# Performance work log

Measured on AMD Instinct MI355X. Metric: run time of the kernel, lower is better.

Reference implementation:

```python
import jax, jax.numpy as jnp
import numpy as np

B, L, E, H = 4, 2048, 512, 8


def setup_inputs() -> dict:
    key = jax.random.key(0)
    ks = jax.random.split(key, 12)
    s = 0.02
    inp = {
        "values": jax.random.normal(ks[0], (B, L, E), jnp.float32),
        "keys": jax.random.normal(ks[1], (B, L, E), jnp.float32),
        "queries": jax.random.normal(ks[2], (B, L, E), jnp.float32),
    }
    mask = jax.random.randint(ks[3], (B, L, H, H), 0, 2, jnp.int32)
    # guarantee at least one unmasked entry per softmax row to avoid NaN rows
    mask = mask.at[..., 0].set(1)
    inp["mask"] = mask
    # Linear(E, E*H) weights stored as (in, out); torch uses y = x @ W.T + b
    inp["Wv"] = jax.random.normal(ks[4], (E, E * H), jnp.float32) * s
    inp["bv"] = jnp.zeros((E * H,), jnp.float32)
    inp["Wk"] = jax.random.normal(ks[5], (E, E * H), jnp.float32) * s
    inp["bk"] = jnp.zeros((E * H,), jnp.float32)
    inp["Wq"] = jax.random.normal(ks[6], (E, E * H), jnp.float32) * s
    inp["bq"] = jnp.zeros((E * H,), jnp.float32)
    inp["Wo"] = jax.random.normal(ks[7], (E * H, E), jnp.float32) * s
    inp["bo"] = jnp.zeros((E,), jnp.float32)
    return inp


def reference(values, keys, queries, mask, Wv, bv, Wk, bk, Wq, bq, Wo, bo):
    b, l, e = queries.shape
    h = Wq.shape[1] // e

    def proj(x, W, bias):
        # (B,L,E) -> (B,L,H,E) -> transpose(1,2) -> (B,H,L,E)
        return (x @ W + bias).reshape(b, -1, h, e).transpose(0, 2, 1, 3)

    v = proj(values, Wv, bv)
    k = proj(keys, Wk, bk)
    q = proj(queries, Wq, bq)
    # Faithful to source: einsum labels applied to the TRANSPOSED (B,H,L,E)
    # tensors, so 'q'/'k' bind to the heads axis and 'h' binds to seq axis.
    # energy: (B, L, H, H) -- head-vs-head scores at each position.
    energy = jnp.einsum('nqhd,nkhd->nhqk', q, k)
    energy = jnp.where(mask == 0, -jnp.inf, energy)
    attn = jax.nn.softmax(energy / jnp.sqrt(jnp.float32(e)), axis=3)
    # out of einsum: (B, H, L, E); raw row-major reshape to (B, L, H*E)
    out = jnp.einsum('nhql,nlhd->nqhd', attn, v).reshape(b, -1, h * e)
    return out @ Wo + bo
```

## Files before the change

### kernel.cpp

```cpp
#include <hip/hip_runtime.h>
#include <stdint.h>

typedef __attribute__((ext_vector_type(4))) float f32x4;
typedef __attribute__((ext_vector_type(8))) __bf16 bf16x8;

__device__ __forceinline__ unsigned short f2bf(float f) {
  union { float f; uint32_t u; } v; v.f = f;
  uint32_t u = v.u;
  return (unsigned short)((u + 0x7FFFu + ((u >> 16) & 1u)) >> 16);
}
__device__ __forceinline__ float bflo(uint32_t u) {
  union { uint32_t u; float f; } v; v.u = u << 16; return v.f;
}
__device__ __forceinline__ float bfhi(uint32_t u) {
  union { uint32_t u; float f; } v; v.u = u & 0xffff0000u; return v.f;
}

__device__ __forceinline__ void async_copy16(void* lds, const void* g) {
  __builtin_amdgcn_global_load_lds(
      (const __attribute__((address_space(1))) void*)g,
      (__attribute__((address_space(3))) void*)lds,
      16, 0, 0);
}

__global__ void cvt3_f32_bf16(const float* __restrict__ in0,
                              const float* __restrict__ in1,
                              const float* __restrict__ in2,
                              uint32_t* __restrict__ out, int n) {
  const float* in = (blockIdx.y == 0) ? in0 : (blockIdx.y == 1) ? in1 : in2;
  uint32_t* o = out + (size_t)blockIdx.y * (n / 2);
  int i = blockIdx.x * blockDim.x + threadIdx.x;
  int idx = i * 8;
  if (idx >= n) return;
  float4 a = *(const float4*)(in + idx);
  float4 b = *(const float4*)(in + idx + 4);
  uint4 ov;
  ov.x = f2bf(a.x) | ((uint32_t)f2bf(a.y) << 16);
  ov.y = f2bf(a.z) | ((uint32_t)f2bf(a.w) << 16);
  ov.z = f2bf(b.x) | ((uint32_t)f2bf(b.y) << 16);
  ov.w = f2bf(b.z) | ((uint32_t)f2bf(b.w) << 16);
  *(uint4*)(o + i * 4) = ov;
}

__global__ void transpose3_to_bf16(const float* __restrict__ in0,
                                   const float* __restrict__ in1,
                                   const float* __restrict__ in2,
                                   unsigned short* __restrict__ out,
                                   int R, int C) {
  const float* in = (blockIdx.z == 0) ? in0 : (blockIdx.z == 1) ? in1 : in2;
  unsigned short* o = out + (size_t)blockIdx.z * ((size_t)R * C);
  __shared__ float tile[32][33];
  int c0 = blockIdx.x * 32, r0 = blockIdx.y * 32;
  int tx = threadIdx.x, ty = threadIdx.y;
  #pragma unroll
  for (int rr = 0; rr < 32; rr += 8)
    tile[ty + rr][tx] = in[(size_t)(r0 + ty + rr) * C + c0 + tx];
  __syncthreads();
  #pragma unroll
  for (int rr = 0; rr < 32; rr += 8)
    o[(size_t)(c0 + ty + rr) * R + r0 + tx] = f2bf(tile[tx][ty + rr]);
}

__global__ void transpose_to_bf16(const float* __restrict__ in,
                                  unsigned short* __restrict__ out,
                                  int R, int C) {
  __shared__ float tile[32][33];
  int c0 = blockIdx.x * 32, r0 = blockIdx.y * 32;
  int tx = threadIdx.x, ty = threadIdx.y;
  #pragma unroll
  for (int rr = 0; rr < 32; rr += 8)
    tile[ty + rr][tx] = in[(size_t)(r0 + ty + rr) * C + c0 + tx];
  __syncthreads();
  #pragma unroll
  for (int rr = 0; rr < 32; rr += 8)
    out[(size_t)(c0 + ty + rr) * R + r0 + tx] = f2bf(tile[tx][ty + rr]);
}

template <int NK, int NN, bool PARTIAL, bool DUAL>
__global__ __launch_bounds__(512, 2) void gemm256(
    const unsigned short* __restrict__ A,
    const unsigned short* __restrict__ Bt,
    const float* __restrict__ bias,
    void* __restrict__ Cout,
    const unsigned short* __restrict__ A2,
    const unsigned short* __restrict__ Bt2,
    const float* __restrict__ bias2,
    void* __restrict__ Cout2,
    int Mt, int NtG, int KC, int Kfull) {
  constexpr int TT = NK * NN;
  static_assert(TT >= 4 && (TT % 2) == 0, "need even TT >= 4");
  __shared__ unsigned short lds[2 * 2 * 256 * 64];

  const int nwg = Mt * NtG * KC;
  const int cpx = nwg >> 3;
  const int bid = blockIdx.x;
  const int nb = (bid & 7) * cpx + (bid >> 3);
  const int kc = nb / (Mt * NtG);
  const int r2 = nb % (Mt * NtG);
  const int bm = r2 / NtG;
  const int ng = r2 % NtG;
  const int mat = DUAL ? (ng >> 3) : 0;
  const int ngm = DUAL ? (ng & 7) : ng;
  const int N = (DUAL ? (NtG >> 1) : NtG) * NN * 256;
  const size_t koff = (size_t)kc * (NK * 64);

  const unsigned short* Asrc = (DUAL && mat) ? A2 : A;
  const unsigned short* Bsrc = (DUAL && mat) ? Bt2 : Bt;
  const float* biasd = (DUAL && mat) ? bias2 : bias;
  void* Cd = (DUAL && mat) ? Cout2 : Cout;

  const int tid = threadIdx.x;
  const int wv = tid >> 6, ln = tid & 63;
  const int wm = wv >> 2, wn = wv & 3;

  f32x4 acc[8][4] = {};
  bf16x8 af[4][2];
  bf16x8 bfb[2][2];

  char* const lds0 = (char*)lds;
  char* const lds1 = (char*)lds + 65536;

  auto stage_tile = [&](int tt, char* dst) {
    const int kt = tt % NK;
    const int bnn = ngm * NN + tt / NK;
    #pragma unroll
    for (int i = 0; i < 4; ++i) {
      const int rb = i * 64 + wv * 8;
      const int row = rb + (ln >> 3);
      const int kcs = (ln & 7) ^ (row & 7);
      async_copy16(dst + rb * 128,
                   Asrc + (size_t)(bm * 256 + row) * Kfull + koff + kt * 64 + kcs * 8);
      async_copy16(dst + 32768 + rb * 128,
                   Bsrc + (size_t)(bnn * 256 + row) * Kfull + koff + kt * 64 + kcs * 8);
    }
  };
  auto load_af = [&](int mh, const char* buf) {
    #pragma unroll
    for (int f = 0; f < 4; ++f) {
      const int lr = wm * 128 + (mh * 4 + f) * 16 + (ln & 15);
      #pragma unroll
      for (int s = 0; s < 2; ++s) {
        const int kq = s * 4 + (ln >> 4);
        af[f][s] = *(const bf16x8*)(buf + lr * 128 + ((kq ^ (lr & 7)) * 16));
      }
    }
  };
  auto load_bf = [&](int nh, const char* buf) {
    #pragma unroll
    for (int gq = 0; gq < 2; ++gq) {
      const int lr = wn * 64 + (nh * 2 + gq) * 16 + (ln & 15);
      #pragma unroll
      for (int s = 0; s < 2; ++s) {
        const int kq = s * 4 + (ln >> 4);
        bfb[gq][s] =
            *(const bf16x8*)(buf + 32768 + lr * 128 + ((kq ^ (lr & 7)) * 16));
      }
    }
  };
  auto mfma_quad = [&](int mh, int nh) {
    #pragma unroll
    for (int s = 0; s < 2; ++s)
      #pragma unroll
      for (int f = 0; f < 4; ++f)
        #pragma unroll
        for (int gq = 0; gq < 2; ++gq)
          acc[mh * 4 + f][nh * 2 + gq] = __builtin_amdgcn_mfma_f32_16x16x32_bf16(
              bfb[gq][s], af[f][s], acc[mh * 4 + f][nh * 2 + gq], 0, 0, 0);
  };
  auto epilogue = [&](int nt) {
    const int m0 = bm * 256 + wm * 128 + (ln & 15);
    const int n0 = (ngm * NN + nt) * 256 + wn * 64 + ((ln >> 4) << 2);
    if (PARTIAL) {
      float* Cp = (float*)Cd + (size_t)kc * ((size_t)Mt * 256) * N;
      #pragma unroll
      for (int f = 0; f < 8; ++f) {
        const int row = m0 + f * 16;
        #pragma unroll
        for (int g = 0; g < 4; ++g)
          *(f32x4*)(Cp + (size_t)row * N + n0 + g * 16) = acc[f][g];
      }
    } else {
      unsigned short* C = (unsigned short*)Cd;
      #pragma unroll
      for (int f = 0; f < 8; ++f) {
        const int row = m0 + f * 16;
        #pragma unroll
        for (int g = 0; g < 4; ++g) {
          const int col = n0 + g * 16;
          float4 bv = *(const float4*)(biasd + col);
          uint2 o;
          o.x = f2bf(acc[f][g][0] + bv.x) | ((uint32_t)f2bf(acc[f][g][1] + bv.y) << 16);
          o.y = f2bf(acc[f][g][2] + bv.z) | ((uint32_t)f2bf(acc[f][g][3] + bv.w) << 16);
          *(uint2*)(C + (size_t)row * N + col) = o;
        }
      }
    }
    #pragma unroll
    for (int f = 0; f < 8; ++f)
      #pragma unroll
      for (int g = 0; g < 4; ++g)
        acc[f][g] = (f32x4){0.f, 0.f, 0.f, 0.f};
  };

  auto tile_body = [&](int tau, const char* buf, char* obuf) {
    if (tau + 1 < TT) stage_tile(tau + 1, obuf);
    load_af(0, buf); load_bf(0, buf);
    mfma_quad(0, 0);
    load_bf(1, buf);
    mfma_quad(0, 1);
    load_af(1, buf);
    mfma_quad(1, 1);
    load_bf(0, buf);
    mfma_quad(1, 0);
    __builtin_amdgcn_sched_barrier(0);
    if (tau + 1 < TT)
      asm volatile("s_waitcnt vmcnt(0)" ::: "memory");
    __builtin_amdgcn_s_barrier();
    if ((tau + 1) % NK == 0) epilogue(tau / NK);
  };

  stage_tile(0, lds0);
  asm volatile("s_waitcnt vmcnt(0)" ::: "memory");
  __builtin_amdgcn_sched_barrier(0);
  __builtin_amdgcn_s_barrier();

  for (int it = 0; it < TT / 2; ++it) {
    tile_body(2 * it,     lds0, lds1);
    tile_body(2 * it + 1, lds1, lds0);
  }
}

__global__ void reduce4_bias(const float* __restrict__ p,
                             const float* __restrict__ bo,
                             float* __restrict__ out) {
  const size_t S = (size_t)8192 * 512;
  size_t i = ((size_t)blockIdx.x * 256 + threadIdx.x) * 4;
  float4 a = *(const float4*)(p + i);
  float4 b = *(const float4*)(p + S + i);
  float4 c = *(const float4*)(p + 2 * S + i);
  float4 d = *(const float4*)(p + 3 * S + i);
  float4 bb = *(const float4*)(bo + (int)(i & 511));
  float4 o;
  o.x = a.x + b.x + c.x + d.x + bb.x;
  o.y = a.y + b.y + c.y + d.y + bb.y;
  o.z = a.z + b.z + c.z + d.z + bb.z;
  o.w = a.w + b.w + c.w + d.w + bb.w;
  *(float4*)(out + i) = o;
}

__global__ __launch_bounds__(256) void energy_mfma(
    const unsigned short* __restrict__ Q,
    const unsigned short* __restrict__ Kb,
    const int* __restrict__ mask,
    float* __restrict__ P) {
  const int wave = threadIdx.x >> 6, ln = threadIdx.x & 63;
  const int t2 = (blockIdx.x * 4 + wave) * 2;
  const int r16 = ln & 15;
  const int g = ln >> 4;
  const size_t rowoff = (size_t)(t2 + (r16 >> 3)) * 4096 + (r16 & 7) * 512 + g * 8;
  const unsigned short* qb = Q + rowoff;
  const unsigned short* kb = Kb + rowoff;

  f32x4 acc = {};
  #pragma unroll
  for (int s = 0; s < 16; ++s) {
    bf16x8 qf = *(const bf16x8*)(qb + s * 32);
    bf16x8 kf = *(const bf16x8*)(kb + s * 32);
    acc = __builtin_amdgcn_mfma_f32_16x16x32_bf16(qf, kf, acc, 0, 0, 0);
  }

  const int ct = r16 >> 3, j = r16 & 7;
  const bool valid = ((g >> 1) == ct);
  const int tok = t2 + ct;
  float pv[4];
  #pragma unroll
  for (int r = 0; r < 4; ++r) {
    const int i = (g & 1) * 4 + r;
    float e = acc[r] * 0.044194173824159216f;
    int mk = 1;
    if (valid) mk = mask[(size_t)tok * 64 + i * 8 + j];
    if (mk == 0) e = -1e30f;
    float m = e;
    m = fmaxf(m, __shfl_xor(m, 1, 64));
    m = fmaxf(m, __shfl_xor(m, 2, 64));
    m = fmaxf(m, __shfl_xor(m, 4, 64));
    float p = __expf(e - m);
    float sum = p;
    sum += __shfl_xor(sum, 1, 64);
    sum += __shfl_xor(sum, 2, 64);
    sum += __shfl_xor(sum, 4, 64);
    pv[r] = p / sum;
  }
  if (valid) {
    #pragma unroll
    for (int r = 0; r < 4; ++r) {
      const int i = (g & 1) * 4 + r;
      P[(size_t)tok * 64 + i * 8 + j] = pv[r];
    }
  }
}

__global__ __launch_bounds__(256) void pv_kernel(
    const float* __restrict__ P,
    const unsigned short* __restrict__ Vb,
    unsigned short* __restrict__ out2) {
  const int wave = threadIdx.x >> 6, lane = threadIdx.x & 63;
  const int t = blockIdx.x * 4 + wave;
  const unsigned short* Vr = Vb + (size_t)t * 4096;
  float att = P[(size_t)t * 64 + lane];

  uint4 v4[8];
  #pragma unroll
  for (int jj = 0; jj < 8; ++jj)
    v4[jj] = *(const uint4*)(Vr + jj * 512 + lane * 8);

  const int nb = t >> 11, l = t & 2047;
  const size_t tok_base = (size_t)nb * 8388608 + (size_t)(l >> 3) * 4096 +
                          (size_t)(l & 7) * 512 + lane * 8;
  #pragma unroll
  for (int hh = 0; hh < 8; ++hh) {
    float accv[8] = {0.f, 0.f, 0.f, 0.f, 0.f, 0.f, 0.f, 0.f};
    #pragma unroll
    for (int jj = 0; jj < 8; ++jj) {
      float a = __shfl(att, hh * 8 + jj, 64);
      accv[0] += a * bflo(v4[jj].x); accv[1] += a * bfhi(v4[jj].x);
      accv[2] += a * bflo(v4[jj].y); accv[3] += a * bfhi(v4[jj].y);
      accv[4] += a * bflo(v4[jj].z); accv[5] += a * bfhi(v4[jj].z);
      accv[6] += a * bflo(v4[jj].w); accv[7] += a * bfhi(v4[jj].w);
    }
    uint4 o;
    o.x = f2bf(accv[0]) | ((uint32_t)f2bf(accv[1]) << 16);
    o.y = f2bf(accv[2]) | ((uint32_t)f2bf(accv[3]) << 16);
    o.z = f2bf(accv[4]) | ((uint32_t)f2bf(accv[5]) << 16);
    o.w = f2bf(accv[6]) | ((uint32_t)f2bf(accv[7]) << 16);
    *(uint4*)(out2 + tok_base + (size_t)hh * 1048576) = o;
  }
}

extern "C" void kernel_launch(void* const* d_in, const int* in_sizes, int n_in,
                              void* d_out, int out_size, void* d_ws, size_t ws_size,
                              hipStream_t stream) {
  const float* values  = (const float*)d_in[0];
  const float* keys    = (const float*)d_in[1];
  const float* queries = (const float*)d_in[2];
  const int*   mask    = (const int*)d_in[3];
  const float* Wv = (const float*)d_in[4];
  const float* bv = (const float*)d_in[5];
  const float* Wk = (const float*)d_in[6];
  const float* bk = (const float*)d_in[7];
  const float* Wq = (const float*)d_in[8];
  const float* bq = (const float*)d_in[9];
  const float* Wo = (const float*)d_in[10];
  const float* bo = (const float*)d_in[11];

  unsigned short* xv  = (unsigned short*)d_ws;
  unsigned short* xk  = xv + 8192 * 512;
  unsigned short* xq  = xk + 8192 * 512;
  unsigned short* Wvt = xq + 8192 * 512;
  unsigned short* Wkt = Wvt + 4096 * 512;
  unsigned short* Wqt = Wkt + 4096 * 512;
  unsigned short* Wot = Wqt + 4096 * 512;
  float*          P   = (float*)(Wot + 4096 * 512);
  unsigned short* bufA = (unsigned short*)(P + 8192 * 64);
  unsigned short* bufB = bufA + (size_t)8192 * 4096;

  const int nx = 8192 * 512;
  cvt3_f32_bf16<<<dim3(nx / 8 / 256, 3), 256, 0, stream>>>(
      values, keys, queries, (uint32_t*)xv, nx);

  transpose3_to_bf16<<<dim3(4096 / 32, 512 / 32, 3), dim3(32, 8), 0, stream>>>(
      Wv, Wk, Wq, Wvt, 512, 4096);
  transpose_to_bf16<<<dim3(512 / 32, 4096 / 32), dim3(32, 8), 0, stream>>>(
      Wo, Wot, 4096, 512);

  gemm256<8, 2, false, true><<<512, 512, 0, stream>>>(
      xq, Wqt, bq, bufA, xk, Wkt, bk, bufB, 32, 16, 1, 512);

  energy_mfma<<<8192 / 8, 256, 0, stream>>>(bufA, bufB, mask, P);

  gemm256<8, 2, false, false><<<256, 512, 0, stream>>>(
      xv, Wvt, bv, bufA, nullptr, nullptr, nullptr, nullptr, 32, 8, 1, 512);

  pv_kernel<<<8192 / 4, 256, 0, stream>>>(P, bufA, bufB);

  gemm256<16, 1, true, false><<<256, 512, 0, stream>>>(
      bufB, Wot, nullptr, (float*)bufA, nullptr, nullptr, nullptr, nullptr,
      32, 2, 4, 4096);
  reduce4_bias<<<4096, 256, 0, stream>>>((float*)bufA, bo, (float*)d_out);
}
```

Measured before the change: 268.6 us.

## Switch GEMM to triple-buffered K=32 tiles with deeper prefetch

The bf16 GEMM moves from a double-buffered 64-wide K tile to a triple-buffered 32-wide K tile. Tiles are prefetched two steps ahead, with a partial vmcnt wait, a new XOR swizzle, and s_setprio around the MFMA block. The QK dual projection now launches 256 workgroups that each cover more N tiles instead of 512. Launch bounds drop to one block per CU, which frees registers for the larger fragment set but lowers occupancy, and the halved K tile doubles the number of barriers per output.

```diff
diff --git a/kernel.cpp b/kernel.cpp
--- a/kernel.cpp
+++ b/kernel.cpp
@@ -77,7 +77,7 @@
 }
 
 template <int NK, int NN, bool PARTIAL, bool DUAL>
-__global__ __launch_bounds__(512, 2) void gemm256(
+__global__ __launch_bounds__(512, 1) void gemm_tb(
     const unsigned short* __restrict__ A,
     const unsigned short* __restrict__ Bt,
     const float* __restrict__ bias,
@@ -88,8 +88,8 @@
     void* __restrict__ Cout2,
     int Mt, int NtG, int KC, int Kfull) {
   constexpr int TT = NK * NN;
-  static_assert(TT >= 4 && (TT % 2) == 0, "need even TT >= 4");
-  __shared__ unsigned short lds[2 * 2 * 256 * 64];
+  static_assert(TT >= 4, "need >=4 tiles");
+  __shared__ unsigned short lds[3 * 2 * 256 * 32];
 
   const int nwg = Mt * NtG * KC;
   const int cpx = nwg >> 3;
@@ -99,10 +99,11 @@
   const int r2 = nb % (Mt * NtG);
   const int bm = r2 / NtG;
   const int ng = r2 % NtG;
-  const int mat = DUAL ? (ng >> 3) : 0;
-  const int ngm = DUAL ? (ng & 7) : ng;
-  const int N = (DUAL ? (NtG >> 1) : NtG) * NN * 256;
-  const size_t koff = (size_t)kc * (NK * 64);
+  const int half = NtG >> 1;
+  const int mat = DUAL ? (ng >= half ? 1 : 0) : 0;
+  const int ngm = DUAL ? (mat ? ng - half : ng) : ng;
+  const int N = (DUAL ? half : NtG) * NN * 256;
+  const size_t koff = (size_t)kc * (NK * 32);
 
   const unsigned short* Asrc = (DUAL && mat) ? A2 : A;
   const unsigned short* Bsrc = (DUAL && mat) ? Bt2 : Bt;
@@ -114,58 +115,34 @@
   const int wm = wv >> 2, wn = wv & 3;
 
   f32x4 acc[8][4] = {};
-  bf16x8 af[4][2];
-  bf16x8 bfb[2][2];
-
-  char* const lds0 = (char*)lds;
-  char* const lds1 = (char*)lds + 65536;
+  bf16x8 af[8];
+  bf16x8 bfb[4];
 
   auto stage_tile = [&](int tt, char* dst) {
     const int kt = tt % NK;
     const int bnn = ngm * NN + tt / NK;
     #pragma unroll
-    for (int i = 0; i < 4; ++i) {
-      const int rb = i * 64 + wv * 8;
-      const int row = rb + (ln >> 3);
-      const int kcs = (ln & 7) ^ (row & 7);
-      async_copy16(dst + rb * 128,
-                   Asrc + (size_t)(bm * 256 + row) * Kfull + koff + kt * 64 + kcs * 8);
-      async_copy16(dst + 32768 + rb * 128,
-                   Bsrc + (size_t)(bnn * 256 + row) * Kfull + koff + kt * 64 + kcs * 8);
+    for (int j = 0; j < 2; ++j) {
+      const int lr = j * 128 + wv * 16 + (ln >> 2);
+      const int srcslot = (ln & 3) ^ ((lr >> 1) & 3);
+      async_copy16(dst + (j * 128 + wv * 16) * 64 + ln * 16,
+                   Asrc + (size_t)(bm * 256 + lr) * Kfull + koff + kt * 32 + srcslot * 8);
+      async_copy16(dst + 16384 + (j * 128 + wv * 16) * 64 + ln * 16,
+                   Bsrc + (size_t)(bnn * 256 + lr) * Kfull + koff + kt * 32 + srcslot * 8);
     }
   };
-  auto load_af = [&](int mh, const char* buf) {
-    #pragma unroll
-    for (int f = 0; f < 4; ++f) {
-      const int lr = wm * 128 + (mh * 4 + f) * 16 + (ln & 15);
-      #pragma unroll
-      for (int s = 0; s < 2; ++s) {
-        const int kq = s * 4 + (ln >> 4);
-        af[f][s] = *(const bf16x8*)(buf + lr * 128 + ((kq ^ (lr & 7)) * 16));
-      }
-    }
-  };
-  auto load_bf = [&](int nh, const char* buf) {
-    #pragma unroll
-    for (int gq = 0; gq < 2; ++gq) {
-      const int lr = wn * 64 + (nh * 2 + gq) * 16 + (ln & 15);
-      #pragma unroll
-      for (int s = 0; s < 2; ++s) {
-        const int kq = s * 4 + (ln >> 4);
-        bfb[gq][s] =
-            *(const bf16x8*)(buf + 32768 + lr * 128 + ((kq ^ (lr & 7)) * 16));
-      }
-    }
-  };
-  auto mfma_quad = [&](int mh, int nh) {
-    #pragma unroll
-    for (int s = 0; s < 2; ++s)
-      #pragma unroll
-      for (int f = 0; f < 4; ++f)
-        #pragma unroll
-        for (int gq = 0; gq < 2; ++gq)
-          acc[mh * 4 + f][nh * 2 + gq] = __builtin_amdgcn_mfma_f32_16x16x32_bf16(
-              bfb[gq][s], af[f][s], acc[mh * 4 + f][nh * 2 + gq], 0, 0, 0);
+  auto load_frags = [&](const char* buf) {
+    const int kq = ln >> 4;
+    #pragma unroll
+    for (int f = 0; f < 8; ++f) {
+      const int lr = wm * 128 + f * 16 + (ln & 15);
+      af[f] = *(const bf16x8*)(buf + lr * 64 + ((kq ^ ((lr >> 1) & 3)) * 16));
+    }
+    #pragma unroll
+    for (int g = 0; g < 4; ++g) {
+      const int lr = wn * 64 + g * 16 + (ln & 15);
+      bfb[g] = *(const bf16x8*)(buf + 16384 + lr * 64 + ((kq ^ ((lr >> 1) & 3)) * 16));
+    }
   };
   auto epilogue = [&](int nt) {
     const int m0 = bm * 256 + wm * 128 + (ln & 15);
@@ -202,31 +179,36 @@
         acc[f][g] = (f32x4){0.f, 0.f, 0.f, 0.f};
   };
 
-  auto tile_body = [&](int tau, const char* buf, char* obuf) {
-    if (tau + 1 < TT) stage_tile(tau + 1, obuf);
-    load_af(0, buf); load_bf(0, buf);
-    mfma_quad(0, 0);
-    load_bf(1, buf);
-    mfma_quad(0, 1);
-    load_af(1, buf);
-    mfma_quad(1, 1);
-    load_bf(0, buf);
-    mfma_quad(1, 0);
-    __builtin_amdgcn_sched_barrier(0);
-    if (tau + 1 < TT)
-      asm volatile("s_waitcnt vmcnt(0)" ::: "memory");
-    __builtin_amdgcn_s_barrier();
-    if ((tau + 1) % NK == 0) epilogue(tau / NK);
-  };
-
-  stage_tile(0, lds0);
-  asm volatile("s_waitcnt vmcnt(0)" ::: "memory");
+  char* b0 = (char*)lds;
+  char* b1 = (char*)lds + 32768;
+  char* b2 = (char*)lds + 65536;
+
+  stage_tile(0, b0);
+  stage_tile(1, b1);
+  asm volatile("s_waitcnt vmcnt(4)" ::: "memory");
   __builtin_amdgcn_sched_barrier(0);
   __builtin_amdgcn_s_barrier();
 
-  for (int it = 0; it < TT / 2; ++it) {
-    tile_body(2 * it,     lds0, lds1);
-    tile_body(2 * it + 1, lds1, lds0);
+  for (int t = 0; t < TT; ++t) {
+    if (t + 2 < TT) stage_tile(t + 2, b2);
+    load_frags(b0);
+    __builtin_amdgcn_s_setprio(1);
+    #pragma unroll
+    for (int f = 0; f < 8; ++f)
+      #pragma unroll
+      for (int g = 0; g < 4; ++g)
+        acc[f][g] = __builtin_amdgcn_mfma_f32_16x16x32_bf16(
+            bfb[g], af[f], acc[f][g], 0, 0, 0);
+    __builtin_amdgcn_s_setprio(0);
+    __builtin_amdgcn_sched_barrier(0);
+    if (t + 2 < TT) {
+      asm volatile("s_waitcnt vmcnt(4)" ::: "memory");
+    } else if (t + 1 < TT) {
+      asm volatile("s_waitcnt vmcnt(0)" ::: "memory");
+    }
+    __builtin_amdgcn_s_barrier();
+    if ((t + 1) % NK == 0) epilogue(t / NK);
+    char* tmp = b0; b0 = b1; b1 = b2; b2 = tmp;
   }
 }
 
@@ -373,17 +355,17 @@
   transpose_to_bf16<<<dim3(512 / 32, 4096 / 32), dim3(32, 8), 0, stream>>>(
       Wo, Wot, 4096, 512);
 
-  gemm256<8, 2, false, true><<<512, 512, 0, stream>>>(
-      xq, Wqt, bq, bufA, xk, Wkt, bk, bufB, 32, 16, 1, 512);
+  gemm_tb<16, 4, false, true><<<256, 512, 0, stream>>>(
+      xq, Wqt, bq, bufA, xk, Wkt, bk, bufB, 32, 8, 1, 512);
 
   energy_mfma<<<8192 / 8, 256, 0, stream>>>(bufA, bufB, mask, P);
 
-  gemm256<8, 2, false, false><<<256, 512, 0, stream>>>(
+  gemm_tb<16, 2, false, false><<<256, 512, 0, stream>>>(
       xv, Wvt, bv, bufA, nullptr, nullptr, nullptr, nullptr, 32, 8, 1, 512);
 
   pv_kernel<<<8192 / 4, 256, 0, stream>>>(P, bufA, bufB);
 
-  gemm256<16, 1, true, false><<<256, 512, 0, stream>>>(
+  gemm_tb<32, 1, true, false><<<256, 512, 0, stream>>>(
       bufB, Wot, nullptr, (float*)bufA, nullptr, nullptr, nullptr, nullptr,
       32, 2, 4, 4096);
   reduce4_bias<<<4096, 256, 0, stream>>>((float*)bufA, bo, (float*)d_out);
```

New measurement: 264.9 us. No clear change (-1.4%).
